# Kernel optimization log

Hardware: AMD Instinct MI355X
Metric: run time of the kernel (lower is better)

The kernel has to match this reference:

```python
import jax, jax.numpy as jnp
import numpy as np

D_MODEL = 512
N_EXPERTS = 8
HIDDEN = D_MODEL * 4
EPS = 1e-10

def setup_inputs() -> dict:
    key = jax.random.key(0)
    ks = jax.random.split(key, 8)
    B, N = 4, 2048
    T = B * N
    x = jax.random.normal(ks[0], (B, N, D_MODEL), dtype=jnp.float32)
    u = jax.random.uniform(ks[1], (T, N_EXPERTS), dtype=jnp.float32, minval=1e-6, maxval=1.0)
    s_in = 1.0 / np.sqrt(D_MODEL)
    s_h = 1.0 / np.sqrt(HIDDEN)
    router_w = jax.random.uniform(ks[2], (D_MODEL, N_EXPERTS), jnp.float32, -s_in, s_in)
    router_b = jax.random.uniform(ks[3], (N_EXPERTS,), jnp.float32, -s_in, s_in)
    w1 = jax.random.uniform(ks[4], (N_EXPERTS, D_MODEL, HIDDEN), jnp.float32, -s_in, s_in)
    b1 = jax.random.uniform(ks[5], (N_EXPERTS, HIDDEN), jnp.float32, -s_in, s_in)
    w2 = jax.random.uniform(ks[6], (N_EXPERTS, HIDDEN, D_MODEL), jnp.float32, -s_h, s_h)
    b2 = jax.random.uniform(ks[7], (N_EXPERTS, D_MODEL), jnp.float32, -s_h, s_h)
    return {"x": x, "u": u, "router_w": router_w, "router_b": router_b,
            "w1": w1, "b1": b1, "w2": w2, "b2": b2}

def reference(x, u, router_w, router_b, w1, b1, w2, b2):
    B, N, d = x.shape
    x_flat = x.reshape(-1, d)  # (T, d)
    logits = x_flat @ router_w + router_b  # (T, E)
    # Gumbel-softmax, tau=1.0, hard=True (straight-through)
    g = -jnp.log(-jnp.log(u) + EPS)
    y_soft = jax.nn.softmax(logits + g, axis=-1)
    idx = jnp.argmax(y_soft, axis=-1)
    hard = jax.nn.one_hot(idx, logits.shape[-1], dtype=y_soft.dtype)
    weights = hard - jax.lax.stop_gradient(y_soft) + y_soft  # (T, E)
    # aux load-balancing loss
    probs = jax.nn.softmax(logits, axis=-1)
    importance = probs.sum(axis=0) / jnp.maximum(jnp.float32(logits.shape[0]), 1.0)
    target = 1.0 / logits.shape[-1]
    aux_loss = jnp.mean((importance - target) ** 2)
    # all-expert dense compute then weighted combine
    h = jax.nn.gelu(jnp.einsum('td,edh->eth', x_flat, w1) + b1[:, None, :], approximate=False)
    expert_outputs = jnp.einsum('eth,ehd->etd', h, w2) + b2[:, None, :]  # (E, T, d)
    output = jnp.einsum('te,etd->td', weights, expert_outputs)
    return output.reshape(B, N, d), aux_loss
```

## Files before the change

### kernel.cpp

```cpp
#include <hip/hip_runtime.h>
#include <stdint.h>
#include <math.h>

#define NUM_TOK 8192
#define DM 512
#define NE 8
#define NH 2048
#define MAX_TILES 72
#define NBLK 32

typedef float f32x4 __attribute__((ext_vector_type(4)));
typedef __bf16 bf16x8 __attribute__((ext_vector_type(8)));

#define WS_COUNTS   0
#define WS_OFFSETS  64
#define WS_CTR      96
#define WS_TILE_E   128
#define WS_TILE_R0  416
#define WS_EXP      704
#define WS_WTOK     33472
#define WS_PERM     66240
#define WS_XG       99008
#define WS_H        8618688
#define WS_W1T      42697408
#define WS_W2T      59474624
#define WS_PROBS    WS_XG
#define WS_BHIST    (WS_H + 32768)
#define WS_BIMP     (WS_H + 33792)

__device__ __forceinline__ uint16_t f2bf(float f) {
  union { float f; uint32_t u; } c; c.f = f;
  return (uint16_t)((c.u + 0x7FFFu + ((c.u >> 16) & 1u)) >> 16);
}

__device__ __forceinline__ float gelu_fast(float v) {
  float z = 1.5957691216f * v * (1.0f + 0.044715f * v * v);
  float em = __expf(-z);
  return v / (1.0f + em);
}

__device__ __forceinline__ void gload_lds16(const void* g, void* l) {
  __builtin_amdgcn_global_load_lds(
      (const __attribute__((address_space(1))) uint32_t*)g,
      (__attribute__((address_space(3))) uint32_t*)l, 16, 0, 0);
}

#define WAIT_BARRIER(N) asm volatile("s_waitcnt vmcnt(" #N ")\ns_barrier" ::: "memory")
#define RAW_BARRIER()   asm volatile("s_barrier" ::: "memory")

__global__ __launch_bounds__(256) void k_prep(
    const float* __restrict__ w1, const float* __restrict__ w2,
    uint16_t* __restrict__ w1t, uint16_t* __restrict__ w2t,
    const float* __restrict__ x, const float* __restrict__ u,
    const float* __restrict__ rw, const float* __restrict__ rb,
    int* __restrict__ expert_of, float* __restrict__ wtok,
    float* __restrict__ probs, int* __restrict__ ctr)
{
  __shared__ float T[64][65];
  int bid = blockIdx.x;

  if (bid == 0 && threadIdx.x == 0)
    __hip_atomic_store(ctr, 0, __ATOMIC_RELAXED, __HIP_MEMORY_SCOPE_AGENT);

  if (bid < 2048) {
    int wv = threadIdx.x >> 6, lane = threadIdx.x & 63;
    int t = bid * 4 + wv;

    const float4* xr = (const float4*)(x + (size_t)t * DM + lane * 8);
    float4 xa = xr[0], xb = xr[1];
    float xs[8] = {xa.x, xa.y, xa.z, xa.w, xb.x, xb.y, xb.z, xb.w};

    double acc[NE];
    #pragma unroll
    for (int e = 0; e < NE; ++e) acc[e] = 0.0;
    #pragma unroll
    for (int j = 0; j < 8; ++j) {
      const float4* rr = (const float4*)(rw + (size_t)(lane * 8 + j) * NE);
      float4 r0 = rr[0], r1 = rr[1];
      double xv = (double)xs[j];
      acc[0] += xv * (double)r0.x; acc[1] += xv * (double)r0.y;
      acc[2] += xv * (double)r0.z; acc[3] += xv * (double)r0.w;
      acc[4] += xv * (double)r1.x; acc[5] += xv * (double)r1.y;
      acc[6] += xv * (double)r1.z; acc[7] += xv * (double)r1.w;
    }
    #pragma unroll
    for (int m = 1; m < 64; m <<= 1) {
      #pragma unroll
      for (int e = 0; e < NE; ++e) acc[e] += __shfl_xor(acc[e], m, 64);
    }
    double lg[NE];
    #pragma unroll
    for (int e = 0; e < NE; ++e) lg[e] = acc[e] + (double)rb[e];

    int le = lane & 7;
    double lgE = le == 0 ? lg[0] : le == 1 ? lg[1] : le == 2 ? lg[2] : le == 3 ? lg[3]
               : le == 4 ? lg[4] : le == 5 ? lg[5] : le == 6 ? lg[6] : lg[7];

    double yE = -1e300;
    if (lane < 8) {
      double uv = (double)u[(size_t)t * NE + lane];
      double g = -log(-log(uv) + 1e-10);
      yE = lgE + g;
    }
    double ymax = yE;
    #pragma unroll
    for (int m = 1; m < 8; m <<= 1) ymax = fmax(ymax, __shfl_xor(ymax, m, 64));
    double ex = (lane < 8) ? exp(yE - ymax) : 0.0;
    double s = ex;
    #pragma unroll
    for (int m = 1; m < 8; m <<= 1) s += __shfl_xor(s, m, 64);
    double p = 1.0 / s;
    unsigned long long mk = __ballot(lane < 8 && yE == ymax);
    int sel = __ffsll(mk) - 1;

    double lm = lgE;
    #pragma unroll
    for (int m = 1; m < 8; m <<= 1) lm = fmax(lm, __shfl_xor(lm, m, 64));
    double pr = exp(lgE - lm);
    double ssum = pr;
    #pragma unroll
    for (int m = 1; m < 8; m <<= 1) ssum += __shfl_xor(ssum, m, 64);

    if (lane < 8) probs[(size_t)t * NE + lane] = (float)(pr / ssum);
    if (lane == 0) {
      expert_of[t] = sel;
      wtok[t] = (float)((1.0 - p) + p);
    }
  } else {
    int id = bid - 2048;
    const float* src; uint16_t* dst; int K, N, nx, rid;
    if (id < 2048) { src = w1; dst = w1t; K = DM; N = NH; nx = NH / 64; rid = id; }
    else           { src = w2; dst = w2t; K = NH; N = DM; nx = DM / 64; rid = id - 2048; }
    int e = rid >> 8;
    int r = rid & 255;
    int n0 = (r % nx) * 64, k0 = (r / nx) * 64;
    const float* sp = src + (size_t)e * K * N;
    uint16_t* d = dst + (size_t)e * K * N;
    int tid = threadIdx.x;
    int tr = tid >> 4;
    int tc = (tid & 15) * 4;
    #pragma unroll
    for (int p = 0; p < 4; ++p) {
      int k = tr + p * 16;
      float4 v = *(const float4*)(sp + (size_t)(k0 + k) * N + n0 + tc);
      T[k][tc] = v.x; T[k][tc + 1] = v.y; T[k][tc + 2] = v.z; T[k][tc + 3] = v.w;
    }
    __syncthreads();
    #pragma unroll
    for (int p = 0; p < 2; ++p) {
      int slot = p * 256 + tid;
      int n = slot >> 3;
      int c = (slot & 7) * 8;
      uint16_t tmp[8];
      #pragma unroll
      for (int j = 0; j < 8; ++j) tmp[j] = f2bf(T[c + j][n]);
      *(uint4*)(d + (size_t)(n0 + n) * K + k0 + c) = *(uint4*)tmp;
    }
  }
}

__global__ __launch_bounds__(256) void k_route2(
    const int* __restrict__ expert_of, const float* __restrict__ probs,
    int* __restrict__ block_hist, float* __restrict__ block_imp,
    int* __restrict__ ctr,
    int* __restrict__ counts, int* __restrict__ offsets,
    float* __restrict__ aux_out, int* __restrict__ tile_e, int* __restrict__ tile_r0,
    int* __restrict__ perm)
{
  __shared__ int whist[4][8];
  __shared__ float wimp[4][8];
  __shared__ int sh[NBLK * 8];
  __shared__ float shf[NBLK * 8];
  __shared__ int scnt[8], soff[8], sbase[8];
  __shared__ float ssum[8];

  int tid = threadIdx.x, lane = tid & 63, wid = tid >> 6;
  int b = blockIdx.x;
  int t = b * 256 + tid;
  int sel = expert_of[t];

  int cnt[8]; int lrank = 0;
  unsigned long long below = (1ull << lane) - 1ull;
  #pragma unroll
  for (int e = 0; e < 8; ++e) {
    unsigned long long m = __ballot(sel == e);
    cnt[e] = (int)__popcll(m);
    if (e == sel) lrank = (int)__popcll(m & below);
  }
  if (lane == 0) {
    #pragma unroll
    for (int e = 0; e < 8; ++e) whist[wid][e] = cnt[e];
  }

  const float4* pp = (const float4*)(probs + (size_t)t * NE);
  float4 pa = pp[0], pb = pp[1];
  float ps[8] = {pa.x, pa.y, pa.z, pa.w, pb.x, pb.y, pb.z, pb.w};
  #pragma unroll
  for (int j = 0; j < 8; ++j) {
    float v = ps[j];
    #pragma unroll
    for (int m = 1; m < 64; m <<= 1) v += __shfl_xor(v, m, 64);
    if (lane == 0) wimp[wid][j] = v;
  }
  __syncthreads();

  if (tid < 8) {
    int c = whist[0][tid] + whist[1][tid] + whist[2][tid] + whist[3][tid];
    __hip_atomic_store(&block_hist[b * 8 + tid], c, __ATOMIC_RELAXED, __HIP_MEMORY_SCOPE_AGENT);
    float sv = wimp[0][tid] + wimp[1][tid] + wimp[2][tid] + wimp[3][tid];
    __hip_atomic_store(&block_imp[b * 8 + tid], sv, __ATOMIC_RELAXED, __HIP_MEMORY_SCOPE_AGENT);
  }
  __syncthreads();

  if (tid == 0) {
    __hip_atomic_fetch_add(ctr, 1, __ATOMIC_RELEASE, __HIP_MEMORY_SCOPE_AGENT);
    while (__hip_atomic_load(ctr, __ATOMIC_ACQUIRE, __HIP_MEMORY_SCOPE_AGENT) < NBLK)
      __builtin_amdgcn_s_sleep(16);
  }
  __syncthreads();

  sh[tid]  = __hip_atomic_load(&block_hist[tid], __ATOMIC_RELAXED, __HIP_MEMORY_SCOPE_AGENT);
  shf[tid] = __hip_atomic_load(&block_imp[tid], __ATOMIC_RELAXED, __HIP_MEMORY_SCOPE_AGENT);
  __syncthreads();

  if (tid < 8) {
    int c = 0; float s = 0.0f;
    #pragma unroll
    for (int bb = 0; bb < NBLK; ++bb) { c += sh[bb * 8 + tid]; s += shf[bb * 8 + tid]; }
    scnt[tid] = c; ssum[tid] = s;
  }
  __syncthreads();
  if (tid < 8) {
    int o = 0;
    for (int e = 0; e < tid; ++e) o += scnt[e];
    soff[tid] = o;
    int run = o;
    for (int bp = 0; bp < b; ++bp) run += sh[bp * 8 + tid];
    sbase[tid] = run;
    if (b == 0) { counts[tid] = scnt[tid]; offsets[tid] = o; }
  }
  __syncthreads();

  if (b == 0 && tid == 0) {
    float a = 0.0f;
    #pragma unroll
    for (int e = 0; e < NE; ++e) {
      float dv = ssum[e] / 8192.0f - 0.125f;
      a += dv * dv;
    }
    aux_out[0] = a / 8.0f;
    int nt = 0;
    for (int e = 0; e < NE; ++e) {
      int ntile = (scnt[e] + 127) >> 7;
      for (int j = 0; j < ntile; ++j) { tile_e[nt] = e; tile_r0[nt] = soff[e] + j * 128; ++nt; }
    }
    for (int i = nt; i < MAX_TILES; ++i) { tile_e[i] = -1; tile_r0[i] = 0; }
  }

  int base = 0;
  #pragma unroll
  for (int w = 0; w < 4; ++w) if (w < wid) base += whist[w][sel];
  perm[sbase[sel] + base + lrank] = t;
}

__global__ __launch_bounds__(64) void k_gather(
    const float* __restrict__ x, const int* __restrict__ perm, uint16_t* __restrict__ Xg)
{
  int r = blockIdx.x;
  int lane = threadIdx.x;
  int t = perm[r];
  const float4* src = (const float4*)(x + (size_t)t * DM);
  float4 a = src[lane * 2];
  float4 b = src[lane * 2 + 1];
  uint32_t p0 = (uint32_t)f2bf(a.x) | ((uint32_t)f2bf(a.y) << 16);
  uint32_t p1 = (uint32_t)f2bf(a.z) | ((uint32_t)f2bf(a.w) << 16);
  uint32_t p2 = (uint32_t)f2bf(b.x) | ((uint32_t)f2bf(b.y) << 16);
  uint32_t p3 = (uint32_t)f2bf(b.z) | ((uint32_t)f2bf(b.w) << 16);
  uint4 v = make_uint4(p0, p1, p2, p3);
  ((uint4*)(Xg + (size_t)r * DM))[lane] = v;
}

__global__ __launch_bounds__(512) void k_ffn1(
    const uint16_t* __restrict__ Xg, const uint16_t* __restrict__ w1t,
    const float* __restrict__ b1,
    const int* __restrict__ offsets, const int* __restrict__ counts,
    const int* __restrict__ tile_e, const int* __restrict__ tile_r0,
    uint16_t* __restrict__ hbuf)
{
  int w = (blockIdx.x & 7) * (MAX_TILES * 16 / 8) + (blockIdx.x >> 3);
  int tile = w >> 4;
  int cb = w & 15;
  int e = tile_e[tile];
  if (e < 0) return;
  int row0 = tile_r0[tile];
  int row_end = offsets[e] + counts[e];
  int n0 = cb * 128;
  const uint16_t* Bt = w1t + (size_t)e * DM * NH;

  __shared__ uint16_t As[2][128 * 64];
  __shared__ uint16_t Bs[2][128 * 64];

  int tid = threadIdx.x;
  int lane = tid & 63, wid = tid >> 6;
  int wm = wid >> 2, wn = wid & 3;
  int l16 = lane & 15, quad = lane >> 4;

  int lrow = lane >> 3;
  int lsw  = (lane & 7) ^ lrow;
  const uint16_t *ga[2], *gb[2];
  int lo[2];
  #pragma unroll
  for (int j = 0; j < 2; ++j) {
    int r = wid * 16 + j * 8;
    ga[j] = Xg + (size_t)(row0 + r + lrow) * DM + lsw * 8;
    gb[j] = Bt + (size_t)(n0 + r + lrow) * DM + lsw * 8;
    lo[j] = r * 64;
  }

  #define FFN1_ISSUE(B) do { \
    _Pragma("unroll") for (int j = 0; j < 2; ++j) { gload_lds16(ga[j], As[B] + lo[j]); ga[j] += 64; } \
    _Pragma("unroll") for (int j = 0; j < 2; ++j) { gload_lds16(gb[j], Bs[B] + lo[j]); gb[j] += 64; } \
  } while (0)

  f32x4 acc[4][2] = {};

  FFN1_ISSUE(0);
  FFN1_ISSUE(1);
  #pragma unroll 2
  for (int k = 0; k < 8; ++k) {
    if (k < 7) WAIT_BARRIER(4); else WAIT_BARRIER(0);
    int b = k & 1;
    const uint16_t* Ab = As[b];
    const uint16_t* Bb = Bs[b];
    #pragma unroll
    for (int ks = 0; ks < 2; ++ks) {
      bf16x8 a[4], bb[2];
      #pragma unroll
      for (int mi = 0; mi < 4; ++mi) {
        int row = wm * 64 + mi * 16 + l16;
        a[mi] = *(const bf16x8*)(Ab + row * 64 + (((ks * 4 + quad) ^ (l16 & 7)) * 8));
      }
      #pragma unroll
      for (int ni = 0; ni < 2; ++ni) {
        int row = wn * 32 + ni * 16 + l16;
        bb[ni] = *(const bf16x8*)(Bb + row * 64 + (((ks * 4 + quad) ^ (l16 & 7)) * 8));
      }
      #pragma unroll
      for (int mi = 0; mi < 4; ++mi)
        #pragma unroll
        for (int ni = 0; ni < 2; ++ni)
          acc[mi][ni] = __builtin_amdgcn_mfma_f32_16x16x32_bf16(a[mi], bb[ni], acc[mi][ni], 0, 0, 0);
    }
    RAW_BARRIER();
    if (k < 6) { if (b) FFN1_ISSUE(1); else FFN1_ISSUE(0); }
  }

  #pragma unroll
  for (int ni = 0; ni < 2; ++ni) {
    int col = n0 + wn * 32 + ni * 16 + l16;
    float bv = b1[e * NH + col];
    #pragma unroll
    for (int mi = 0; mi < 4; ++mi) {
      int rbase = wm * 64 + mi * 16 + quad * 4;
      #pragma unroll
      for (int r = 0; r < 4; ++r) {
        int grow = row0 + rbase + r;
        if (grow < row_end) {
          float v = acc[mi][ni][r] + bv;
          hbuf[(size_t)grow * NH + col] = f2bf(gelu_fast(v));
        }
      }
    }
  }
}

__global__ __launch_bounds__(512) void k_ffn2(
    const uint16_t* __restrict__ hbuf, const uint16_t* __restrict__ w2t,
    const float* __restrict__ b2,
    const int* __restrict__ offsets, const int* __restrict__ counts,
    const int* __restrict__ tile_e, const int* __restrict__ tile_r0,
    const int* __restrict__ perm, const float* __restrict__ wtok,
    float* __restrict__ out)
{
  int w = (blockIdx.x & 7) * (MAX_TILES * 8 / 8) + (blockIdx.x >> 3);
  int tile = w >> 3;
  int cb = w & 7;
  int e = tile_e[tile];
  if (e < 0) return;
  int row0 = tile_r0[tile];
  int row_end = offsets[e] + counts[e];
  int n0 = cb * 64;
  const uint16_t* Bt = w2t + (size_t)e * NH * DM;

  __shared__ uint16_t As[2][128 * 64];
  __shared__ uint16_t Bs[2][64 * 64];

  int tid = threadIdx.x;
  int lane = tid & 63, wid = tid >> 6;
  int wm = wid >> 1, wn = wid & 1;
  int l16 = lane & 15, quad = lane >> 4;

  int lrow = lane >> 3;
  int lsw  = (lane & 7) ^ lrow;
  const uint16_t *ga[2], *gb;
  int loa[2], lob;
  #pragma unroll
  for (int j = 0; j < 2; ++j) {
    int r = wid * 16 + j * 8;
    ga[j] = hbuf + (size_t)(row0 + r + lrow) * NH + lsw * 8;
    loa[j] = r * 64;
  }
  {
    int r = wid * 8;
    gb = Bt + (size_t)(n0 + r + lrow) * NH + lsw * 8;
    lob = r * 64;
  }

  #define FFN2_ISSUE(B) do { \
    _Pragma("unroll") for (int j = 0; j < 2; ++j) { gload_lds16(ga[j], As[B] + loa[j]); ga[j] += 64; } \
    gload_lds16(gb, Bs[B] + lob); gb += 64; \
  } while (0)

  f32x4 acc[2][2] = {};

  FFN2_ISSUE(0);
  FFN2_ISSUE(1);
  #pragma unroll 2
  for (int k = 0; k < 32; ++k) {
    if (k < 31) WAIT_BARRIER(3); else WAIT_BARRIER(0);
    int b = k & 1;
    const uint16_t* Ab = As[b];
    const uint16_t* Bb = Bs[b];
    #pragma unroll
    for (int ks = 0; ks < 2; ++ks) {
      bf16x8 a[2], bb[2];
      #pragma unroll
      for (int mi = 0; mi < 2; ++mi) {
        int row = wm * 32 + mi * 16 + l16;
        a[mi] = *(const bf16x8*)(Ab + row * 64 + (((ks * 4 + quad) ^ (l16 & 7)) * 8));
      }
      #pragma unroll
      for (int ni = 0; ni < 2; ++ni) {
        int row = wn * 32 + ni * 16 + l16;
        bb[ni] = *(const bf16x8*)(Bb + row * 64 + (((ks * 4 + quad) ^ (l16 & 7)) * 8));
      }
      #pragma unroll
      for (int mi = 0; mi < 2; ++mi)
        #pragma unroll
        for (int ni = 0; ni < 2; ++ni)
          acc[mi][ni] = __builtin_amdgcn_mfma_f32_16x16x32_bf16(a[mi], bb[ni], acc[mi][ni], 0, 0, 0);
    }
    RAW_BARRIER();
    if (k < 30) { if (b) FFN2_ISSUE(1); else FFN2_ISSUE(0); }
  }

  #pragma unroll
  for (int ni = 0; ni < 2; ++ni) {
    int col = n0 + wn * 32 + ni * 16 + l16;
    float bv = b2[e * DM + col];
    #pragma unroll
    for (int mi = 0; mi < 2; ++mi) {
      int rbase = wm * 32 + mi * 16 + quad * 4;
      #pragma unroll
      for (int r = 0; r < 4; ++r) {
        int grow = row0 + rbase + r;
        if (grow < row_end) {
          int tk = perm[grow];
          float wt = wtok[tk];
          out[(size_t)tk * DM + col] = (acc[mi][ni][r] + bv) * wt;
        }
      }
    }
  }
}

extern "C" void kernel_launch(void* const* d_in, const int* in_sizes, int n_in,
                              void* d_out, int out_size, void* d_ws, size_t ws_size,
                              hipStream_t stream)
{
  const float* x  = (const float*)d_in[0];
  const float* u  = (const float*)d_in[1];
  const float* rw = (const float*)d_in[2];
  const float* rb = (const float*)d_in[3];
  const float* w1 = (const float*)d_in[4];
  const float* b1 = (const float*)d_in[5];
  const float* w2 = (const float*)d_in[6];
  const float* b2 = (const float*)d_in[7];
  float* out = (float*)d_out;

  char* ws = (char*)d_ws;
  int*      counts     = (int*)(ws + WS_COUNTS);
  int*      offsets    = (int*)(ws + WS_OFFSETS);
  int*      ctr        = (int*)(ws + WS_CTR);
  int*      tile_e     = (int*)(ws + WS_TILE_E);
  int*      tile_r0    = (int*)(ws + WS_TILE_R0);
  int*      expert_of  = (int*)(ws + WS_EXP);
  float*    wtok       = (float*)(ws + WS_WTOK);
  int*      perm       = (int*)(ws + WS_PERM);
  float*    probs      = (float*)(ws + WS_PROBS);
  int*      block_hist = (int*)(ws + WS_BHIST);
  float*    block_imp  = (float*)(ws + WS_BIMP);
  uint16_t* Xg         = (uint16_t*)(ws + WS_XG);
  uint16_t* hbuf       = (uint16_t*)(ws + WS_H);
  uint16_t* w1t        = (uint16_t*)(ws + WS_W1T);
  uint16_t* w2t        = (uint16_t*)(ws + WS_W2T);

  k_prep<<<dim3(6144), 256, 0, stream>>>(w1, w2, w1t, w2t, x, u, rw, rb,
                                         expert_of, wtok, probs, ctr);
  k_route2<<<dim3(NBLK), 256, 0, stream>>>(expert_of, probs, block_hist, block_imp, ctr,
                                           counts, offsets, out + (size_t)NUM_TOK * DM,
                                           tile_e, tile_r0, perm);
  k_gather<<<dim3(NUM_TOK), 64, 0, stream>>>(x, perm, Xg);
  k_ffn1<<<dim3(MAX_TILES * 16), 512, 0, stream>>>(Xg, w1t, b1, offsets, counts, tile_e, tile_r0, hbuf);
  k_ffn2<<<dim3(MAX_TILES * 8), 512, 0, stream>>>(hbuf, w2t, b2, offsets, counts, tile_e, tile_r0, perm, wtok, out);
}
```

Baseline: 253.9 us.

## Enlarge expert GEMM tiles to 256x128 with triple-buffered LDS pipeline

Row tiles for each expert grow from 128 to 256 tokens, and FFN2 column blocks grow from 64 to 128. Both FFN kernels now share one 3-stage LDS-buffered loop body. That loop splits the next-stage loads across the MFMA sub-steps and raises wave priority around MFMA issue. Larger tiles improve operand reuse and cut the number of weight reloads. The cost is more padding waste on partial expert tiles, fewer blocks (160 for FFN2) which may underfill the CUs, and higher LDS and register use.

```diff
diff --git a/kernel.cpp b/kernel.cpp
--- a/kernel.cpp
+++ b/kernel.cpp
@@ -6,7 +6,7 @@
 #define DM 512
 #define NE 8
 #define NH 2048
-#define MAX_TILES 72
+#define MAX_TILES 40
 #define NBLK 32
 
 typedef float f32x4 __attribute__((ext_vector_type(4)));
@@ -251,8 +251,8 @@
     aux_out[0] = a / 8.0f;
     int nt = 0;
     for (int e = 0; e < NE; ++e) {
-      int ntile = (scnt[e] + 127) >> 7;
-      for (int j = 0; j < ntile; ++j) { tile_e[nt] = e; tile_r0[nt] = soff[e] + j * 128; ++nt; }
+      int ntile = (scnt[e] + 255) >> 8;
+      for (int j = 0; j < ntile; ++j) { tile_e[nt] = e; tile_r0[nt] = soff[e] + j * 256; ++nt; }
     }
     for (int i = nt; i < MAX_TILES; ++i) { tile_e[i] = -1; tile_r0[i] = 0; }
   }
@@ -280,6 +280,95 @@
   ((uint4*)(Xg + (size_t)r * DM))[lane] = v;
 }
 
+
+#define ISS_A01(AS, B) { gload_lds16(ga[0], AS[B] + loa[0]); ga[0] += 64; \
+                         gload_lds16(ga[1], AS[B] + loa[1]); ga[1] += 64; }
+#define ISS_A23(AS, B) { gload_lds16(ga[2], AS[B] + loa[2]); ga[2] += 64; \
+                         gload_lds16(ga[3], AS[B] + loa[3]); ga[3] += 64; }
+#define ISS_B01(BS, B) { gload_lds16(gb[0], BS[B] + lob[0]); gb[0] += 64; \
+                         gload_lds16(gb[1], BS[B] + lob[1]); gb[1] += 64; }
+
+#define FFN_TILE_BODY(AS, BS, KT)                                              \
+  for (int t = 0; t < KT; ++t) {                                               \
+    if (t < KT - 1) WAIT_BARRIER(6); else WAIT_BARRIER(0);                     \
+    int bsel = t % 3;                                                          \
+    const uint16_t* Ab = &AS[bsel][0];                                         \
+    const uint16_t* Bb = &BS[bsel][0];                                         \
+    int nb = (t + 2) % 3;                                                      \
+    bool st = (t < KT - 2);                                                    \
+    int xo0 = (quad ^ (l16 & 7)) * 8;                                          \
+    int xo1 = ((4 + quad) ^ (l16 & 7)) * 8;                                    \
+                                            \
+    bf16x8 bb0[2], bb1[2];                                                     \
+    _Pragma("unroll")                                                          \
+    for (int ni = 0; ni < 2; ++ni)                                             \
+      bb0[ni] = *(const bf16x8*)(Bb + (wn * 32 + ni * 16 + l16) * 64 + xo0);   \
+    {                                                                          \
+      bf16x8 a[4];                                                             \
+      _Pragma("unroll")                                                        \
+      for (int mi = 0; mi < 4; ++mi)                                           \
+        a[mi] = *(const bf16x8*)(Ab + (wm * 128 + mi * 16 + l16) * 64 + xo0);  \
+      if (st) ISS_A01(AS, nb);                                                 \
+      __builtin_amdgcn_s_setprio(1);                                           \
+      _Pragma("unroll")                                                        \
+      for (int mi = 0; mi < 4; ++mi)                                           \
+        _Pragma("unroll")                                                      \
+        for (int ni = 0; ni < 2; ++ni)                                         \
+          acc[mi][ni] = __builtin_amdgcn_mfma_f32_16x16x32_bf16(a[mi], bb0[ni], acc[mi][ni], 0, 0, 0); \
+      __builtin_amdgcn_s_setprio(0);                                           \
+    }                                                                          \
+    RAW_BARRIER();                                                             \
+                                                     \
+    {                                                                          \
+      bf16x8 a[4];                                                             \
+      _Pragma("unroll")                                                        \
+      for (int mi = 0; mi < 4; ++mi)                                           \
+        a[mi] = *(const bf16x8*)(Ab + (wm * 128 + (mi + 4) * 16 + l16) * 64 + xo0); \
+      if (st) ISS_A23(AS, nb);                                                 \
+      __builtin_amdgcn_s_setprio(1);                                           \
+      _Pragma("unroll")                                                        \
+      for (int mi = 0; mi < 4; ++mi)                                           \
+        _Pragma("unroll")                                                      \
+        for (int ni = 0; ni < 2; ++ni)                                         \
+          acc[mi + 4][ni] = __builtin_amdgcn_mfma_f32_16x16x32_bf16(a[mi], bb0[ni], acc[mi + 4][ni], 0, 0, 0); \
+      __builtin_amdgcn_s_setprio(0);                                           \
+    }                                                                          \
+    RAW_BARRIER();                                                             \
+                                            \
+    _Pragma("unroll")                                                          \
+    for (int ni = 0; ni < 2; ++ni)                                             \
+      bb1[ni] = *(const bf16x8*)(Bb + (wn * 32 + ni * 16 + l16) * 64 + xo1);   \
+    {                                                                          \
+      bf16x8 a[4];                                                             \
+      _Pragma("unroll")                                                        \
+      for (int mi = 0; mi < 4; ++mi)                                           \
+        a[mi] = *(const bf16x8*)(Ab + (wm * 128 + mi * 16 + l16) * 64 + xo1);  \
+      if (st) ISS_B01(BS, nb);                                                 \
+      __builtin_amdgcn_s_setprio(1);                                           \
+      _Pragma("unroll")                                                        \
+      for (int mi = 0; mi < 4; ++mi)                                           \
+        _Pragma("unroll")                                                      \
+        for (int ni = 0; ni < 2; ++ni)                                         \
+          acc[mi][ni] = __builtin_amdgcn_mfma_f32_16x16x32_bf16(a[mi], bb1[ni], acc[mi][ni], 0, 0, 0); \
+      __builtin_amdgcn_s_setprio(0);                                           \
+    }                                                                          \
+    RAW_BARRIER();                                                             \
+          \
+    {                                                                          \
+      bf16x8 a[4];                                                             \
+      _Pragma("unroll")                                                        \
+      for (int mi = 0; mi < 4; ++mi)                                           \
+        a[mi] = *(const bf16x8*)(Ab + (wm * 128 + (mi + 4) * 16 + l16) * 64 + xo1); \
+      __builtin_amdgcn_s_setprio(1);                                           \
+      _Pragma("unroll")                                                        \
+      for (int mi = 0; mi < 4; ++mi)                                           \
+        _Pragma("unroll")                                                      \
+        for (int ni = 0; ni < 2; ++ni)                                         \
+          acc[mi + 4][ni] = __builtin_amdgcn_mfma_f32_16x16x32_bf16(a[mi], bb1[ni], acc[mi + 4][ni], 0, 0, 0); \
+      __builtin_amdgcn_s_setprio(0);                                           \
+    }                                                                          \
+  }
+
 __global__ __launch_bounds__(512) void k_ffn1(
     const uint16_t* __restrict__ Xg, const uint16_t* __restrict__ w1t,
     const float* __restrict__ b1,
@@ -287,9 +376,8 @@
     const int* __restrict__ tile_e, const int* __restrict__ tile_r0,
     uint16_t* __restrict__ hbuf)
 {
-  int w = (blockIdx.x & 7) * (MAX_TILES * 16 / 8) + (blockIdx.x >> 3);
-  int tile = w >> 4;
-  int cb = w & 15;
+  int w = (blockIdx.x & 7) * (640 / 8) + (blockIdx.x >> 3);
+  int tile = w >> 4, cb = w & 15;
   int e = tile_e[tile];
   if (e < 0) return;
   int row0 = tile_r0[tile];
@@ -297,71 +385,47 @@
   int n0 = cb * 128;
   const uint16_t* Bt = w1t + (size_t)e * DM * NH;
 
-  __shared__ uint16_t As[2][128 * 64];
-  __shared__ uint16_t Bs[2][128 * 64];
+  __shared__ uint16_t As[3][256 * 64];
+  __shared__ uint16_t Bs[3][128 * 64];
 
   int tid = threadIdx.x;
   int lane = tid & 63, wid = tid >> 6;
   int wm = wid >> 2, wn = wid & 3;
   int l16 = lane & 15, quad = lane >> 4;
-
   int lrow = lane >> 3;
   int lsw  = (lane & 7) ^ lrow;
-  const uint16_t *ga[2], *gb[2];
-  int lo[2];
+
+  const uint16_t *ga[4], *gb[2];
+  int loa[4], lob[2];
+  #pragma unroll
+  for (int j = 0; j < 4; ++j) {
+    int rbase = wid * 32 + j * 8;
+    int rr = row0 + rbase + lrow;
+    if (rr > NUM_TOK + 127) rr = NUM_TOK + 127;
+    ga[j] = Xg + (size_t)rr * DM + lsw * 8;
+    loa[j] = rbase * 64;
+  }
   #pragma unroll
   for (int j = 0; j < 2; ++j) {
-    int r = wid * 16 + j * 8;
-    ga[j] = Xg + (size_t)(row0 + r + lrow) * DM + lsw * 8;
-    gb[j] = Bt + (size_t)(n0 + r + lrow) * DM + lsw * 8;
-    lo[j] = r * 64;
-  }
-
-  #define FFN1_ISSUE(B) do { \
-    _Pragma("unroll") for (int j = 0; j < 2; ++j) { gload_lds16(ga[j], As[B] + lo[j]); ga[j] += 64; } \
-    _Pragma("unroll") for (int j = 0; j < 2; ++j) { gload_lds16(gb[j], Bs[B] + lo[j]); gb[j] += 64; } \
-  } while (0)
-
-  f32x4 acc[4][2] = {};
-
-  FFN1_ISSUE(0);
-  FFN1_ISSUE(1);
-  #pragma unroll 2
-  for (int k = 0; k < 8; ++k) {
-    if (k < 7) WAIT_BARRIER(4); else WAIT_BARRIER(0);
-    int b = k & 1;
-    const uint16_t* Ab = As[b];
-    const uint16_t* Bb = Bs[b];
-    #pragma unroll
-    for (int ks = 0; ks < 2; ++ks) {
-      bf16x8 a[4], bb[2];
-      #pragma unroll
-      for (int mi = 0; mi < 4; ++mi) {
-        int row = wm * 64 + mi * 16 + l16;
-        a[mi] = *(const bf16x8*)(Ab + row * 64 + (((ks * 4 + quad) ^ (l16 & 7)) * 8));
-      }
-      #pragma unroll
-      for (int ni = 0; ni < 2; ++ni) {
-        int row = wn * 32 + ni * 16 + l16;
-        bb[ni] = *(const bf16x8*)(Bb + row * 64 + (((ks * 4 + quad) ^ (l16 & 7)) * 8));
-      }
-      #pragma unroll
-      for (int mi = 0; mi < 4; ++mi)
-        #pragma unroll
-        for (int ni = 0; ni < 2; ++ni)
-          acc[mi][ni] = __builtin_amdgcn_mfma_f32_16x16x32_bf16(a[mi], bb[ni], acc[mi][ni], 0, 0, 0);
-    }
-    RAW_BARRIER();
-    if (k < 6) { if (b) FFN1_ISSUE(1); else FFN1_ISSUE(0); }
-  }
+    int rbase = wid * 16 + j * 8;
+    gb[j] = Bt + (size_t)(n0 + rbase + lrow) * DM + lsw * 8;
+    lob[j] = rbase * 64;
+  }
+
+  f32x4 acc[8][2] = {};
+
+  ISS_A01(As, 0); ISS_A23(As, 0); ISS_B01(Bs, 0);
+  ISS_A01(As, 1); ISS_A23(As, 1); ISS_B01(Bs, 1);
+
+  FFN_TILE_BODY(As, Bs, 8)
 
   #pragma unroll
   for (int ni = 0; ni < 2; ++ni) {
     int col = n0 + wn * 32 + ni * 16 + l16;
     float bv = b1[e * NH + col];
     #pragma unroll
-    for (int mi = 0; mi < 4; ++mi) {
-      int rbase = wm * 64 + mi * 16 + quad * 4;
+    for (int mi = 0; mi < 8; ++mi) {
+      int rbase = wm * 128 + mi * 16 + quad * 4;
       #pragma unroll
       for (int r = 0; r < 4; ++r) {
         int grow = row0 + rbase + r;
@@ -382,85 +446,56 @@
     const int* __restrict__ perm, const float* __restrict__ wtok,
     float* __restrict__ out)
 {
-  int w = (blockIdx.x & 7) * (MAX_TILES * 8 / 8) + (blockIdx.x >> 3);
-  int tile = w >> 3;
-  int cb = w & 7;
+  int w = (blockIdx.x & 7) * (160 / 8) + (blockIdx.x >> 3);
+  int tile = w >> 2, cb = w & 3;
   int e = tile_e[tile];
   if (e < 0) return;
   int row0 = tile_r0[tile];
   int row_end = offsets[e] + counts[e];
-  int n0 = cb * 64;
+  int n0 = cb * 128;
   const uint16_t* Bt = w2t + (size_t)e * NH * DM;
 
-  __shared__ uint16_t As[2][128 * 64];
-  __shared__ uint16_t Bs[2][64 * 64];
+  __shared__ uint16_t As[3][256 * 64];
+  __shared__ uint16_t Bs[3][128 * 64];
 
   int tid = threadIdx.x;
   int lane = tid & 63, wid = tid >> 6;
-  int wm = wid >> 1, wn = wid & 1;
+  int wm = wid >> 2, wn = wid & 3;
   int l16 = lane & 15, quad = lane >> 4;
-
   int lrow = lane >> 3;
   int lsw  = (lane & 7) ^ lrow;
-  const uint16_t *ga[2], *gb;
-  int loa[2], lob;
+
+  const uint16_t *ga[4], *gb[2];
+  int loa[4], lob[2];
+  #pragma unroll
+  for (int j = 0; j < 4; ++j) {
+    int rbase = wid * 32 + j * 8;
+    int rr = row0 + rbase + lrow;
+    if (rr > NUM_TOK + 127) rr = NUM_TOK + 127;
+    ga[j] = hbuf + (size_t)rr * NH + lsw * 8;
+    loa[j] = rbase * 64;
+  }
   #pragma unroll
   for (int j = 0; j < 2; ++j) {
-    int r = wid * 16 + j * 8;
-    ga[j] = hbuf + (size_t)(row0 + r + lrow) * NH + lsw * 8;
-    loa[j] = r * 64;
-  }
-  {
-    int r = wid * 8;
-    gb = Bt + (size_t)(n0 + r + lrow) * NH + lsw * 8;
-    lob = r * 64;
-  }
-
-  #define FFN2_ISSUE(B) do { \
-    _Pragma("unroll") for (int j = 0; j < 2; ++j) { gload_lds16(ga[j], As[B] + loa[j]); ga[j] += 64; } \
-    gload_lds16(gb, Bs[B] + lob); gb += 64; \
-  } while (0)
-
-  f32x4 acc[2][2] = {};
-
-  FFN2_ISSUE(0);
-  FFN2_ISSUE(1);
-  #pragma unroll 2
-  for (int k = 0; k < 32; ++k) {
-    if (k < 31) WAIT_BARRIER(3); else WAIT_BARRIER(0);
-    int b = k & 1;
-    const uint16_t* Ab = As[b];
-    const uint16_t* Bb = Bs[b];
-    #pragma unroll
-    for (int ks = 0; ks < 2; ++ks) {
-      bf16x8 a[2], bb[2];
-      #pragma unroll
-      for (int mi = 0; mi < 2; ++mi) {
-        int row = wm * 32 + mi * 16 + l16;
-        a[mi] = *(const bf16x8*)(Ab + row * 64 + (((ks * 4 + quad) ^ (l16 & 7)) * 8));
-      }
-      #pragma unroll
-      for (int ni = 0; ni < 2; ++ni) {
-        int row = wn * 32 + ni * 16 + l16;
-        bb[ni] = *(const bf16x8*)(Bb + row * 64 + (((ks * 4 + quad) ^ (l16 & 7)) * 8));
-      }
-      #pragma unroll
-      for (int mi = 0; mi < 2; ++mi)
-        #pragma unroll
-        for (int ni = 0; ni < 2; ++ni)
-          acc[mi][ni] = __builtin_amdgcn_mfma_f32_16x16x32_bf16(a[mi], bb[ni], acc[mi][ni], 0, 0, 0);
-    }
-    RAW_BARRIER();
-    if (k < 30) { if (b) FFN2_ISSUE(1); else FFN2_ISSUE(0); }
-  }
+    int rbase = wid * 16 + j * 8;
+    gb[j] = Bt + (size_t)(n0 + rbase + lrow) * NH + lsw * 8;
+    lob[j] = rbase * 64;
+  }
+
+  f32x4 acc[8][2] = {};
+
+  ISS_A01(As, 0); ISS_A23(As, 0); ISS_B01(Bs, 0);
+  ISS_A01(As, 1); ISS_A23(As, 1); ISS_B01(Bs, 1);
+
+  FFN_TILE_BODY(As, Bs, 32)
 
   #pragma unroll
   for (int ni = 0; ni < 2; ++ni) {
     int col = n0 + wn * 32 + ni * 16 + l16;
     float bv = b2[e * DM + col];
     #pragma unroll
-    for (int mi = 0; mi < 2; ++mi) {
-      int rbase = wm * 32 + mi * 16 + quad * 4;
+    for (int mi = 0; mi < 8; ++mi) {
+      int rbase = wm * 128 + mi * 16 + quad * 4;
       #pragma unroll
       for (int r = 0; r < 4; ++r) {
         int grow = row0 + rbase + r;
@@ -511,6 +546,6 @@
                                            counts, offsets, out + (size_t)NUM_TOK * DM,
                                            tile_e, tile_r0, perm);
   k_gather<<<dim3(NUM_TOK), 64, 0, stream>>>(x, perm, Xg);
-  k_ffn1<<<dim3(MAX_TILES * 16), 512, 0, stream>>>(Xg, w1t, b1, offsets, counts, tile_e, tile_r0, hbuf);
-  k_ffn2<<<dim3(MAX_TILES * 8), 512, 0, stream>>>(hbuf, w2t, b2, offsets, counts, tile_e, tile_r0, perm, wtok, out);
-}
+  k_ffn1<<<dim3(640), 512, 0, stream>>>(Xg, w1t, b1, offsets, counts, tile_e, tile_r0, hbuf);
+  k_ffn2<<<dim3(160), 512, 0, stream>>>(hbuf, w2t, b2, offsets, counts, tile_e, tile_r0, perm, wtok, out);
+}
```

New measurement: 292.5 us. 1.15x slower.
